# Optimization experiments

Measured on AMD Instinct MI355X. Metric: run time of the kernel, lower is better.

## Reference

```python
import jax, jax.numpy as jnp
import numpy as np

H, DH = 8, 16  # num_heads, head_dim (out_feats // num_heads)
NP, NA, NS = 100000, 60000, 1000


def _gat_conv(feat_src, feat_dst, n_dst, src, dst, W, al, ar, b):
    # DGL GATConv (eval mode: feat_drop/attn_drop are identity)
    hs = (feat_src @ W).reshape(-1, H, DH)          # [Ns,H,D]
    hd = (feat_dst @ W).reshape(-1, H, DH)          # [Nd,H,D]
    el = (hs * al).sum(-1)                          # [Ns,H]
    er = (hd * ar).sum(-1)                          # [Nd,H]
    e = jax.nn.leaky_relu(el[src] + er[dst], negative_slope=0.2)  # [E,H]
    # segment softmax over edges sharing a destination node
    emax = jax.ops.segment_max(e, dst, num_segments=n_dst)
    emax = jnp.where(jnp.isfinite(emax), emax, 0.0)
    ee = jnp.exp(e - emax[dst])
    denom = jax.ops.segment_sum(ee, dst, num_segments=n_dst)
    alpha = ee / jnp.maximum(denom[dst], 1e-9)      # [E,H]
    m = jax.ops.segment_sum(alpha[:, :, None] * hs[src], dst, num_segments=n_dst)
    return m.reshape(n_dst, H * DH) + b             # [Nd, out_feats]


def setup_inputs() -> dict:
    key = jax.random.key(0)
    ks = jax.random.split(key, 18)
    Epa, Eps = 300000, 150000
    f32 = jnp.float32
    inp = {
        "feat_paper_0": jax.random.normal(ks[0], (NP, 128), f32),
        "feat_author_0": jax.random.normal(ks[1], (NA, 128), f32),
        "feat_subject_0": jax.random.normal(ks[2], (NS, 128), f32),
        "feat_paper_1": jax.random.normal(ks[3], (NP, 128), f32),
        "feat_author_1": jax.random.normal(ks[4], (NA, 128), f32),
        "feat_subject_1": jax.random.normal(ks[5], (NS, 128), f32),
        "pa_src": jax.random.randint(ks[6], (Epa,), 0, NP, jnp.int32),
        "pa_dst": jax.random.randint(ks[7], (Epa,), 0, NA, jnp.int32),
        "ap_src": jax.random.randint(ks[8], (Epa,), 0, NA, jnp.int32),
        "ap_dst": jax.random.randint(ks[9], (Epa,), 0, NP, jnp.int32),
        "ps_src": jax.random.randint(ks[10], (Eps,), 0, NP, jnp.int32),
        "ps_dst": jax.random.randint(ks[11], (Eps,), 0, NS, jnp.int32),
        "sp_src": jax.random.randint(ks[12], (Eps,), 0, NS, jnp.int32),
        "sp_dst": jax.random.randint(ks[13], (Eps,), 0, NP, jnp.int32),
        "Ws": jax.random.normal(ks[14], (4, 128, 128), f32) * 0.08,
        "als": jax.random.normal(ks[15], (4, H, DH), f32) * 0.1,
        "ars": jax.random.normal(ks[16], (4, H, DH), f32) * 0.1,
        "bs": jnp.zeros((4, 128), f32),
    }
    return inp


def reference(feat_paper_0, feat_author_0, feat_subject_0,
              feat_paper_1, feat_author_1, feat_subject_1,
              pa_src, pa_dst, ap_src, ap_dst, ps_src, ps_dst, sp_src, sp_dst,
              Ws, als, ars, bs):
    def one_input(fp, fa, fs):
        # rel 0: paper->author, 1: author->paper, 2: paper->subject, 3: subject->paper
        h_author = _gat_conv(fp, fa, NA, pa_src, pa_dst, Ws[0], als[0], ars[0], bs[0])
        h_paper_ap = _gat_conv(fa, fp, NP, ap_src, ap_dst, Ws[1], als[1], ars[1], bs[1])
        h_subject = _gat_conv(fp, fs, NS, ps_src, ps_dst, Ws[2], als[2], ars[2], bs[2])
        h_paper_sp = _gat_conv(fs, fp, NP, sp_src, sp_dst, Ws[3], als[3], ars[3], bs[3])
        h_paper = (h_paper_ap + h_paper_sp) * 0.5  # HeteroGraphConv aggregate='mean'
        # act = identity; key order for ACM: [paper, author, subject]
        return jnp.concatenate([h_paper, h_author, h_subject], axis=0)

    out0 = one_input(feat_paper_0, feat_author_0, feat_subject_0)
    out1 = one_input(feat_paper_1, feat_author_1, feat_subject_1)
    return jnp.stack([out0, out1], axis=0)  # [2, NP+NA+NS, 128]
```

## Files before the change

### kernel.cpp

```cpp
#include <hip/hip_runtime.h>

#define NHEAD 8
#define NPAPER 100000
#define NAUTHOR 60000
#define NSUBJ 1000
#define NTOT (NPAPER + NAUTHOR + NSUBJ)
#define NDEG 261000

typedef __attribute__((ext_vector_type(8))) short bf16x8;
typedef __attribute__((ext_vector_type(4))) float f32x4;

__device__ __forceinline__ unsigned short f2bf(float x) {
    unsigned int u = __builtin_bit_cast(unsigned int, x);
    u += 0x7fffu + ((u >> 16) & 1u);
    return (unsigned short)(u >> 16);
}
__device__ __forceinline__ float bf2f_lo(unsigned int v) {
    return __builtin_bit_cast(float, v << 16);
}
__device__ __forceinline__ float bf2f_hi(unsigned int v) {
    return __builtin_bit_cast(float, v & 0xffff0000u);
}

__global__ void prep_kernel(const float* __restrict__ Ws, const float* __restrict__ als,
                            const float* __restrict__ ars,
                            unsigned short* __restrict__ Wt,
                            unsigned short* __restrict__ combo, int* __restrict__ deg) {
    int b = blockIdx.x;
    if (b >= 288) {
        int idx = (b - 288) * 1024 + threadIdx.x * 4;
        if (idx < NDEG) *reinterpret_cast<int4*>(&deg[idx]) = int4{0, 0, 0, 0};
        return;
    }
    int idx = b * 256 + threadIdx.x;
    if (idx < 65536) {
        int r = idx >> 14, rem = idx & 16383, c = rem >> 7, k = rem & 127;
        Wt[idx] = f2bf(Ws[(r << 14) + k * 128 + c]);
    } else if (idx < 65536 + 8192) {
        int j = idx - 65536;
        int r = j >> 11, rem = j & 2047, n = rem >> 7, k = rem & 127;
        int p = r ^ 1;
        const float *W, *a;
        if (n < 8) {
            W = Ws + (r << 14) + k * 128 + n * 16;
            a = als + r * 128 + n * 16;
        } else {
            int h = n - 8;
            W = Ws + (p << 14) + k * 128 + h * 16;
            a = ars + p * 128 + h * 16;
        }
        float s = 0.f;
#pragma unroll
        for (int d = 0; d < 16; ++d) s += W[d] * a[d];
        combo[j] = f2bf(s);
    }
}

__device__ __forceinline__ void stage_W(unsigned short* Wl, const unsigned short* Wt,
                                        const unsigned short* cb, int tid) {
#pragma unroll
    for (int it = 0; it < 9; ++it) {
        int id = it * 256 + tid;
        int r = id >> 4, c8 = id & 15;
        const unsigned short* srcp = (r < 128) ? (Wt + r * 128) : (cb + (r - 128) * 128);
        uint4 v = *reinterpret_cast<const uint4*>(srcp + c8 * 8);
        *reinterpret_cast<uint4*>(&Wl[(r * 16 + (c8 ^ (r & 15))) * 8]) = v;
    }
}

__device__ __forceinline__ void mfma_set(const unsigned short* Wl, unsigned short* Abf,
                                         const bf16x8* af, int tid, int row0, int N,
                                         float* __restrict__ el, float* __restrict__ er) {
    const int l = tid & 63, w = tid >> 6, lrow = l & 15, lk8 = l >> 4;
#pragma unroll
    for (int t9 = 0; t9 < 9; ++t9) {
        f32x4 acc = f32x4{0.f, 0.f, 0.f, 0.f};
#pragma unroll
        for (int ks = 0; ks < 4; ++ks) {
            int wrow = t9 * 16 + lrow;
            int c8 = ks * 4 + lk8;
            bf16x8 bf = *reinterpret_cast<const bf16x8*>(
                &Wl[(wrow * 16 + (c8 ^ (wrow & 15))) * 8]);
            acc = __builtin_amdgcn_mfma_f32_16x16x32_bf16(af[ks], bf, acc, 0, 0, 0);
        }
        if (t9 < 8) {
#pragma unroll
            for (int r = 0; r < 4; ++r) {
                int rl = w * 16 + lk8 * 4 + r;
                int col = t9 * 16 + lrow;
                Abf[(rl * 16 + ((col >> 3) ^ (rl & 15))) * 8 + (col & 7)] = f2bf(acc[r]);
            }
        } else {
#pragma unroll
            for (int r = 0; r < 4; ++r) {
                int row = row0 + w * 16 + lk8 * 4 + r;
                if (row < N) {
                    if (lrow < 8) el[(size_t)row * 8 + lrow] = acc[r];
                    else er[(size_t)row * 8 + (lrow - 8)] = acc[r];
                }
            }
        }
    }
}

__device__ __forceinline__ void store_hs(const unsigned short* Abf,
                                         unsigned short* __restrict__ hs, int tid,
                                         int row0, int N) {
#pragma unroll
    for (int it = 0; it < 4; ++it) {
        int id = it * 256 + tid;
        int r = id >> 4, c8 = id & 15;
        int row = row0 + r;
        if (row < N) {
            uint4 v = *reinterpret_cast<const uint4*>(&Abf[(r * 16 + (c8 ^ (r & 15))) * 8]);
            *reinterpret_cast<uint4*>(hs + (size_t)row * 128 + c8 * 8) = v;
        }
    }
}

struct PCArgs {
    const int* edst[4];
    int ebase[5];
    int nbase[4];
    int* deg;
    int cblk;
    const float* A[6];
    int N[6];
    int blk0[7];
    const unsigned short* Wt1[6];
    const unsigned short* cb1[6];
    unsigned short* hs1[6];
    float* el1[6];
    float* er1[6];
    const unsigned short* Wt2[6];
    const unsigned short* cb2[6];
    unsigned short* hs2[6];
    float* el2[6];
    float* er2[6];
    int has2[6];
};

__global__ __launch_bounds__(256) void project_count(PCArgs a) {
    __shared__ unsigned short Abf[64 * 128];
    __shared__ unsigned short Wl[144 * 128];
    int bb = blockIdx.x;
    const int tid = threadIdx.x;
    if (bb < a.cblk) {
        int idx = bb * 256 + tid;
        if (idx < a.ebase[4]) {
            int r = 0;
            while (idx >= a.ebase[r + 1]) ++r;
            atomicAdd(&a.deg[a.nbase[r] + a.edst[r][idx - a.ebase[r]]], 1);
        }
        return;
    }
    bb -= a.cblk;
    int t = 0;
    while (bb >= a.blk0[t + 1]) ++t;
    const int row0 = (bb - a.blk0[t]) * 64;
    const int N = a.N[t];
    const float* A = a.A[t];

#pragma unroll
    for (int it = 0; it < 4; ++it) {
        int id = it * 256 + tid;
        int r = id >> 4, c8 = id & 15;
        int row = row0 + r;
        if (row >= N) row = N - 1;
        const float4* ap = reinterpret_cast<const float4*>(A + (size_t)row * 128 + c8 * 8);
        float4 v0 = ap[0], v1 = ap[1];
        uint4 pk;
        pk.x = (unsigned)f2bf(v0.x) | ((unsigned)f2bf(v0.y) << 16);
        pk.y = (unsigned)f2bf(v0.z) | ((unsigned)f2bf(v0.w) << 16);
        pk.z = (unsigned)f2bf(v1.x) | ((unsigned)f2bf(v1.y) << 16);
        pk.w = (unsigned)f2bf(v1.z) | ((unsigned)f2bf(v1.w) << 16);
        *reinterpret_cast<uint4*>(&Abf[(r * 16 + (c8 ^ (r & 15))) * 8]) = pk;
    }
    stage_W(Wl, a.Wt1[t], a.cb1[t], tid);
    __syncthreads();

    const int l = tid & 63, w = tid >> 6, lrow = l & 15, lk8 = l >> 4;
    bf16x8 af[4];
    const int arow = w * 16 + lrow;
#pragma unroll
    for (int ks = 0; ks < 4; ++ks) {
        int c8 = ks * 4 + lk8;
        af[ks] = *reinterpret_cast<const bf16x8*>(
            &Abf[(arow * 16 + (c8 ^ (arow & 15))) * 8]);
    }
    __syncthreads();

    mfma_set(Wl, Abf, af, tid, row0, N, a.el1[t], a.er1[t]);
    __syncthreads();
    store_hs(Abf, a.hs1[t], tid, row0, N);
    if (!a.has2[t]) return;
    stage_W(Wl, a.Wt2[t], a.cb2[t], tid);
    __syncthreads();
    mfma_set(Wl, Abf, af, tid, row0, N, a.el2[t], a.er2[t]);
    __syncthreads();
    store_hs(Abf, a.hs2[t], tid, row0, N);
}

__global__ __launch_bounds__(256) void scan_bsum(const int* __restrict__ deg,
                                                 int* __restrict__ bsums, int N) {
    int base = blockIdx.x * 1024 + threadIdx.x * 4;
    int s = 0;
#pragma unroll
    for (int j = 0; j < 4; ++j) {
        int i = base + j;
        if (i < N) s += deg[i];
    }
#pragma unroll
    for (int off = 32; off; off >>= 1) s += __shfl_down(s, off);
    __shared__ int wt[4];
    if ((threadIdx.x & 63) == 0) wt[threadIdx.x >> 6] = s;
    __syncthreads();
    if (threadIdx.x == 0) bsums[blockIdx.x] = wt[0] + wt[1] + wt[2] + wt[3];
}

__global__ __launch_bounds__(256) void scan_final(const int* __restrict__ deg,
                                                  const int* __restrict__ bsums,
                                                  int* __restrict__ row_ptr,
                                                  int* __restrict__ cursor, int N) {
    int t = threadIdx.x;
    __shared__ int s_start;
    __shared__ int wsum[4];
    {
        int acc = 0;
        for (int i = t; i < (int)blockIdx.x; i += 256) acc += bsums[i];
#pragma unroll
        for (int off = 32; off; off >>= 1) acc += __shfl_down(acc, off);
        if ((t & 63) == 0) wsum[t >> 6] = acc;
        __syncthreads();
        if (t == 0) s_start = wsum[0] + wsum[1] + wsum[2] + wsum[3];
        __syncthreads();
    }
    int base = blockIdx.x * 1024 + t * 4;
    int d[4];
    int s = 0;
#pragma unroll
    for (int j = 0; j < 4; ++j) {
        int i = base + j;
        d[j] = (i < N) ? deg[i] : 0;
        s += d[j];
    }
    int inc = s;
#pragma unroll
    for (int off = 1; off < 64; off <<= 1) {
        int u = __shfl_up(inc, off);
        if ((t & 63) >= off) inc += u;
    }
    __shared__ int wt[4];
    if ((t & 63) == 63) wt[t >> 6] = inc;
    __syncthreads();
    int start = s_start;
    for (int w = 0; w < (t >> 6); ++w) start += wt[w];
    start += inc - s;
#pragma unroll
    for (int j = 0; j < 4; ++j) {
        int i = base + j;
        if (i < N) {
            row_ptr[i] = start;
            cursor[i] = start;
        }
        start += d[j];
    }
    if (base < N && base + 4 >= N) row_ptr[N] = start;
}

struct CsrPtrs {
    const int* esrc[4];
    const int* edst[4];
    int ebase[5];
    int nbase[4];
};

__global__ void csr_scatter(CsrPtrs cp, int* __restrict__ cursor,
                            int* __restrict__ srcs) {
    int idx = blockIdx.x * 256 + threadIdx.x;
    if (idx >= cp.ebase[4]) return;
    int r = 0;
    while (idx >= cp.ebase[r + 1]) ++r;
    int e = idx - cp.ebase[r];
    int p = atomicAdd(&cursor[cp.nbase[r] + cp.edst[r][e]], 1);
    srcs[p] = cp.esrc[r][e];
}

__device__ __forceinline__ void acc_list(int p0, int p1, float erd, int l, int h,
                                         const int* __restrict__ srcs,
                                         const float* __restrict__ el,
                                         const unsigned short* __restrict__ hs,
                                         float* A, float& DS) {
    float a4[4][8];
    float dv[4] = {0.f, 0.f, 0.f, 0.f};
#pragma unroll
    for (int u = 0; u < 4; ++u)
#pragma unroll
        for (int j = 0; j < 8; ++j) a4[u][j] = 0.f;
    int p = p0;
    for (; p + 4 <= p1; p += 4) {
        int sx[4];
#pragma unroll
        for (int u = 0; u < 4; ++u) sx[u] = srcs[p + u];
        float ev[4];
        uint4 q[4];
#pragma unroll
        for (int u = 0; u < 4; ++u) {
            ev[u] = el[(size_t)sx[u] * 8 + h] + erd;
            q[u] = *reinterpret_cast<const uint4*>(hs + (size_t)sx[u] * 128 + l * 8);
        }
#pragma unroll
        for (int u = 0; u < 4; ++u) {
            float e = ev[u];
            e = e > 0.f ? e : 0.2f * e;
            float ee = __expf(e);
            dv[u] += ee;
            a4[u][0] += ee * bf2f_lo(q[u].x);
            a4[u][1] += ee * bf2f_hi(q[u].x);
            a4[u][2] += ee * bf2f_lo(q[u].y);
            a4[u][3] += ee * bf2f_hi(q[u].y);
            a4[u][4] += ee * bf2f_lo(q[u].z);
            a4[u][5] += ee * bf2f_hi(q[u].z);
            a4[u][6] += ee * bf2f_lo(q[u].w);
            a4[u][7] += ee * bf2f_hi(q[u].w);
        }
    }
    for (; p < p1; ++p) {
        int s = srcs[p];
        float e = el[(size_t)s * 8 + h] + erd;
        e = e > 0.f ? e : 0.2f * e;
        float ee = __expf(e);
        uint4 q = *reinterpret_cast<const uint4*>(hs + (size_t)s * 128 + l * 8);
        dv[0] += ee;
        a4[0][0] += ee * bf2f_lo(q.x);
        a4[0][1] += ee * bf2f_hi(q.x);
        a4[0][2] += ee * bf2f_lo(q.y);
        a4[0][3] += ee * bf2f_hi(q.y);
        a4[0][4] += ee * bf2f_lo(q.z);
        a4[0][5] += ee * bf2f_hi(q.z);
        a4[0][6] += ee * bf2f_lo(q.w);
        a4[0][7] += ee * bf2f_hi(q.w);
    }
#pragma unroll
    for (int j = 0; j < 8; ++j) A[j] = a4[0][j] + a4[1][j] + a4[2][j] + a4[3][j];
    DS = dv[0] + dv[1] + dv[2] + dv[3];
}

#define PB 12500
#define AB 7500
#define SB 2000

struct AggArgs {
    const int* rp;
    const int* srcs;
    const float* el[8];
    const float* er[8];
    const unsigned short* hs[8];
    const float* bs;
    float* out0;
    float* out1;
};

__global__ __launch_bounds__(256) void mega_agg(AggArgs a) {
    int blk = blockIdx.x;
    __shared__ float Am[16][128];
    __shared__ float Dm[16][8];

    if (blk < PB) {
        int g = blk * 16 + (threadIdx.x >> 4);
        int l = threadIdx.x & 15, h = l >> 1;
        int inp = g >= NPAPER;
        int dst = inp ? g - NPAPER : g;
        float* out = (inp ? a.out1 : a.out0) + (size_t)dst * 128 + l * 8;
        float A1[8], A3[8], d1, d3;
        acc_list(a.rp[60000 + dst], a.rp[60000 + dst + 1],
                 a.er[inp * 4 + 1][(size_t)dst * 8 + h], l, h, a.srcs,
                 a.el[inp * 4 + 1], a.hs[inp * 4 + 1], A1, d1);
        acc_list(a.rp[161000 + dst], a.rp[161000 + dst + 1],
                 a.er[inp * 4 + 3][(size_t)dst * 8 + h], l, h, a.srcs,
                 a.el[inp * 4 + 3], a.hs[inp * 4 + 3], A3, d3);
        float i1 = 1.f / fmaxf(d1, 1e-9f);
        float i3 = 1.f / fmaxf(d3, 1e-9f);
        const float4* bp1 = reinterpret_cast<const float4*>(a.bs + 128 + l * 8);
        const float4* bp3 = reinterpret_cast<const float4*>(a.bs + 384 + l * 8);
        float4 b10 = bp1[0], b11 = bp1[1], b30 = bp3[0], b31 = bp3[1];
        float4 o0, o1;
        o0.x = 0.5f * ((A1[0] * i1 + b10.x) + (A3[0] * i3 + b30.x));
        o0.y = 0.5f * ((A1[1] * i1 + b10.y) + (A3[1] * i3 + b30.y));
        o0.z = 0.5f * ((A1[2] * i1 + b10.z) + (A3[2] * i3 + b30.z));
        o0.w = 0.5f * ((A1[3] * i1 + b10.w) + (A3[3] * i3 + b30.w));
        o1.x = 0.5f * ((A1[4] * i1 + b11.x) + (A3[4] * i3 + b31.x));
        o1.y = 0.5f * ((A1[5] * i1 + b11.y) + (A3[5] * i3 + b31.y));
        o1.z = 0.5f * ((A1[6] * i1 + b11.z) + (A3[6] * i3 + b31.z));
        o1.w = 0.5f * ((A1[7] * i1 + b11.w) + (A3[7] * i3 + b31.w));
        reinterpret_cast<float4*>(out)[0] = o0;
        reinterpret_cast<float4*>(out)[1] = o1;
    } else if (blk < PB + AB) {
        int g = (blk - PB) * 16 + (threadIdx.x >> 4);
        int l = threadIdx.x & 15, h = l >> 1;
        int inp = g >= NAUTHOR;
        int dst = inp ? g - NAUTHOR : g;
        float* out = (inp ? a.out1 : a.out0) + (size_t)(NPAPER + dst) * 128 + l * 8;
        float A[8], ds;
        acc_list(a.rp[dst], a.rp[dst + 1], a.er[inp * 4 + 0][(size_t)dst * 8 + h], l, h,
                 a.srcs, a.el[inp * 4 + 0], a.hs[inp * 4 + 0], A, ds);
        float inv = 1.f / fmaxf(ds, 1e-9f);
        const float4* bp = reinterpret_cast<const float4*>(a.bs + l * 8);
        float4 b0 = bp[0], b1 = bp[1];
        float4 o0 = make_float4(A[0] * inv + b0.x, A[1] * inv + b0.y,
                                A[2] * inv + b0.z, A[3] * inv + b0.w);
        float4 o1 = make_float4(A[4] * inv + b1.x, A[5] * inv + b1.y,
                                A[6] * inv + b1.z, A[7] * inv + b1.w);
        reinterpret_cast<float4*>(out)[0] = o0;
        reinterpret_cast<float4*>(out)[1] = o1;
    } else {
        int b2 = blk - (PB + AB);
        int inp = b2 >= NSUBJ;
        int dst = inp ? b2 - NSUBJ : b2;
        const float* el = a.el[inp * 4 + 2];
        const float* er = a.er[inp * 4 + 2];
        const unsigned short* hs = a.hs[inp * 4 + 2];
        float* out = (inp ? a.out1 : a.out0) + (size_t)(NPAPER + NAUTHOR + dst) * 128;
        int gl = threadIdx.x >> 4;
        int l = threadIdx.x & 15, h = l >> 1;
        int p0 = a.rp[160000 + dst], p1 = a.rp[160000 + dst + 1];
        float erd = er[(size_t)dst * 8 + h];
        float acc8[8];
#pragma unroll
        for (int j = 0; j < 8; ++j) acc8[j] = 0.f;
        float dsum = 0.f;
        for (int p = p0 + gl; p < p1; p += 16) {
            int s = a.srcs[p];
            float e = el[(size_t)s * 8 + h] + erd;
            e = e > 0.f ? e : 0.2f * e;
            float ee = __expf(e);
            uint4 q = *reinterpret_cast<const uint4*>(hs + (size_t)s * 128 + l * 8);
            dsum += ee;
            acc8[0] += ee * bf2f_lo(q.x);
            acc8[1] += ee * bf2f_hi(q.x);
            acc8[2] += ee * bf2f_lo(q.y);
            acc8[3] += ee * bf2f_hi(q.y);
            acc8[4] += ee * bf2f_lo(q.z);
            acc8[5] += ee * bf2f_hi(q.z);
            acc8[6] += ee * bf2f_lo(q.w);
            acc8[7] += ee * bf2f_hi(q.w);
        }
#pragma unroll
        for (int j = 0; j < 8; ++j) Am[gl][l * 8 + j] = acc8[j];
        if ((l & 1) == 0) Dm[gl][h] = dsum;
        __syncthreads();
        int c = threadIdx.x;
        if (c < 128) {
            float s = 0.f, dn = 0.f;
            int hh = c >> 4;
#pragma unroll
            for (int g = 0; g < 16; ++g) {
                s += Am[g][c];
                dn += Dm[g][hh];
            }
            out[c] = s / fmaxf(dn, 1e-9f) + a.bs[256 + c];
        }
    }
}

extern "C" void kernel_launch(void* const* d_in, const int* in_sizes, int n_in,
                              void* d_out, int out_size, void* d_ws, size_t ws_size,
                              hipStream_t stream) {
    const float* Ws4 = (const float*)d_in[14];
    const float* als = (const float*)d_in[15];
    const float* ars = (const float*)d_in[16];
    const float* bs = (const float*)d_in[17];
    float* out = (float*)d_out;

    const int Es[4] = {in_sizes[6], in_sizes[8], in_sizes[10], in_sizes[12]};
    const int Nsrcs[4] = {NPAPER, NAUTHOR, NPAPER, NSUBJ};
    const int Ndsts[4] = {NAUTHOR, NPAPER, NSUBJ, NPAPER};
    const int Etot = Es[0] + Es[1] + Es[2] + Es[3];

    char* wsp = (char*)d_ws;
    auto carve = [&](size_t bytes) {
        char* p = wsp;
        wsp += (bytes + 255) & ~(size_t)255;
        return p;
    };
    unsigned short* Wt = (unsigned short*)carve(4 * 16384 * 2);
    unsigned short* combo = (unsigned short*)carve(4 * 2048 * 2);
    unsigned short* hsb[2][4];
    float* elb[2][4];
    float* erb[2][4];
    for (int i = 0; i < 2; ++i)
        for (int r = 0; r < 4; ++r) {
            hsb[i][r] = (unsigned short*)carve((size_t)Nsrcs[r] * 128 * 2);
            elb[i][r] = (float*)carve((size_t)Nsrcs[r] * 8 * 4);
            erb[i][r] = (float*)carve((size_t)Ndsts[r] * 8 * 4);
        }
    int* deg = (int*)carve((size_t)NDEG * 4);
    int* cursor = (int*)carve((size_t)NDEG * 4);
    int* bsums = (int*)carve(1024);
    int* rp = (int*)carve((size_t)(NDEG + 1) * 4);
    int* scsr = (int*)carve((size_t)Etot * 4);

    prep_kernel<<<288 + (NDEG + 1023) / 1024, 256, 0, stream>>>(Ws4, als, ars, Wt,
                                                                combo, deg);

    PCArgs pc;
    pc.edst[0] = (const int*)d_in[7];
    pc.edst[1] = (const int*)d_in[9];
    pc.edst[2] = (const int*)d_in[11];
    pc.edst[3] = (const int*)d_in[13];
    pc.ebase[0] = 0;
    for (int r = 0; r < 4; ++r) pc.ebase[r + 1] = pc.ebase[r] + Es[r];
    pc.nbase[0] = 0;
    pc.nbase[1] = 60000;
    pc.nbase[2] = 160000;
    pc.nbase[3] = 161000;
    pc.deg = deg;
    pc.cblk = (Etot + 255) / 256;

    int blk = 0;
    for (int ti = 0; ti < 6; ++ti) {
        int i = ti & 1;
        int nodeT = ti >> 1;
        const int relOf[3] = {0, 1, 3};
        int r = relOf[nodeT];
        const float* feats[3] = {(const float*)d_in[0 + 3 * i],
                                 (const float*)d_in[1 + 3 * i],
                                 (const float*)d_in[2 + 3 * i]};
        pc.A[ti] = feats[nodeT];
        pc.N[ti] = (nodeT == 0) ? NPAPER : (nodeT == 1 ? NAUTHOR : NSUBJ);
        pc.blk0[ti] = blk;
        blk += (pc.N[ti] + 63) / 64;
        pc.Wt1[ti] = Wt + (size_t)r * 16384;
        pc.cb1[ti] = combo + (size_t)r * 2048;
        pc.hs1[ti] = hsb[i][r];
        pc.el1[ti] = elb[i][r];
        pc.er1[ti] = erb[i][r ^ 1];
        pc.has2[ti] = (nodeT == 0);
        int r2 = 2;
        pc.Wt2[ti] = Wt + (size_t)r2 * 16384;
        pc.cb2[ti] = combo + (size_t)r2 * 2048;
        pc.hs2[ti] = hsb[i][r2];
        pc.el2[ti] = elb[i][r2];
        pc.er2[ti] = erb[i][r2 ^ 1];
    }
    pc.blk0[6] = blk;
    project_count<<<pc.cblk + blk, 256, 0, stream>>>(pc);

    int nb = (NDEG + 1023) / 1024;
    scan_bsum<<<nb, 256, 0, stream>>>(deg, bsums, NDEG);
    scan_final<<<nb, 256, 0, stream>>>(deg, bsums, rp, cursor, NDEG);

    CsrPtrs cp;
    cp.esrc[0] = (const int*)d_in[6];  cp.edst[0] = (const int*)d_in[7];
    cp.esrc[1] = (const int*)d_in[8];  cp.edst[1] = (const int*)d_in[9];
    cp.esrc[2] = (const int*)d_in[10]; cp.edst[2] = (const int*)d_in[11];
    cp.esrc[3] = (const int*)d_in[12]; cp.edst[3] = (const int*)d_in[13];
    for (int r = 0; r < 5; ++r) cp.ebase[r] = pc.ebase[r];
    for (int r = 0; r < 4; ++r) cp.nbase[r] = pc.nbase[r];
    csr_scatter<<<(Etot + 255) / 256, 256, 0, stream>>>(cp, cursor, scsr);

    AggArgs ag;
    ag.rp = rp;
    ag.srcs = scsr;
    for (int i = 0; i < 2; ++i)
        for (int r = 0; r < 4; ++r) {
            ag.el[i * 4 + r] = elb[i][r];
            ag.er[i * 4 + r] = erb[i][r];
            ag.hs[i * 4 + r] = hsb[i][r];
        }
    ag.bs = bs;
    ag.out0 = out;
    ag.out1 = out + (size_t)NTOT * 128;
    mega_agg<<<PB + AB + SB, 256, 0, stream>>>(ag);
}
```

Measured before the change: 384.0 us.

## Process both inputs per destination in one pass sharing CSR source indices

The aggregation kernel now handles inputs 0 and 1 together for each destination node, so each CSR source index and row pointer is loaded once and feeds two gathers. The unroll-by-4 partial accumulators are replaced with two accumulator sets, one per input. The subject path splits the block into two 8-group halves, one per input, and the block count is halved. Non-temporal loads and stores are added for feature reads and output writes. More loads are in flight per thread, but the kernel now uses more registers and each accumulator has fewer independent chains.

```diff
diff --git a/kernel.cpp b/kernel.cpp
--- a/kernel.cpp
+++ b/kernel.cpp
@@ -9,6 +9,7 @@
 
 typedef __attribute__((ext_vector_type(8))) short bf16x8;
 typedef __attribute__((ext_vector_type(4))) float f32x4;
+typedef __attribute__((ext_vector_type(4))) unsigned int u32x4;
 
 __device__ __forceinline__ unsigned short f2bf(float x) {
     unsigned int u = __builtin_bit_cast(unsigned int, x);
@@ -167,8 +168,9 @@
         int r = id >> 4, c8 = id & 15;
         int row = row0 + r;
         if (row >= N) row = N - 1;
-        const float4* ap = reinterpret_cast<const float4*>(A + (size_t)row * 128 + c8 * 8);
-        float4 v0 = ap[0], v1 = ap[1];
+        const f32x4* ap = reinterpret_cast<const f32x4*>(A + (size_t)row * 128 + c8 * 8);
+        f32x4 v0 = __builtin_nontemporal_load(ap);
+        f32x4 v1 = __builtin_nontemporal_load(ap + 1);
         uint4 pk;
         pk.x = (unsigned)f2bf(v0.x) | ((unsigned)f2bf(v0.y) << 16);
         pk.y = (unsigned)f2bf(v0.z) | ((unsigned)f2bf(v0.w) << 16);
@@ -286,69 +288,102 @@
     srcs[p] = cp.esrc[r][e];
 }
 
-__device__ __forceinline__ void acc_list(int p0, int p1, float erd, int l, int h,
-                                         const int* __restrict__ srcs,
-                                         const float* __restrict__ el,
-                                         const unsigned short* __restrict__ hs,
-                                         float* A, float& DS) {
-    float a4[4][8];
-    float dv[4] = {0.f, 0.f, 0.f, 0.f};
-#pragma unroll
-    for (int u = 0; u < 4; ++u)
-#pragma unroll
-        for (int j = 0; j < 8; ++j) a4[u][j] = 0.f;
+__device__ __forceinline__ void acc_dual(
+    int p0, int p1, float erd0, float erd1, int l, int h,
+    const int* __restrict__ srcs,
+    const float* __restrict__ el0, const float* __restrict__ el1,
+    const unsigned short* __restrict__ hs0, const unsigned short* __restrict__ hs1,
+    float* A0, float* A1, float& DS0, float& DS1) {
+    float a0[8], a1[8];
+#pragma unroll
+    for (int j = 0; j < 8; ++j) { a0[j] = 0.f; a1[j] = 0.f; }
+    float d0 = 0.f, d1 = 0.f;
     int p = p0;
     for (; p + 4 <= p1; p += 4) {
         int sx[4];
 #pragma unroll
         for (int u = 0; u < 4; ++u) sx[u] = srcs[p + u];
-        float ev[4];
-        uint4 q[4];
+        float ev0[4], ev1[4];
+        uint4 q0[4], q1[4];
 #pragma unroll
         for (int u = 0; u < 4; ++u) {
-            ev[u] = el[(size_t)sx[u] * 8 + h] + erd;
-            q[u] = *reinterpret_cast<const uint4*>(hs + (size_t)sx[u] * 128 + l * 8);
+            ev0[u] = el0[(size_t)sx[u] * 8 + h] + erd0;
+            ev1[u] = el1[(size_t)sx[u] * 8 + h] + erd1;
+            q0[u] = *reinterpret_cast<const uint4*>(hs0 + (size_t)sx[u] * 128 + l * 8);
+            q1[u] = *reinterpret_cast<const uint4*>(hs1 + (size_t)sx[u] * 128 + l * 8);
         }
 #pragma unroll
         for (int u = 0; u < 4; ++u) {
-            float e = ev[u];
-            e = e > 0.f ? e : 0.2f * e;
-            float ee = __expf(e);
-            dv[u] += ee;
-            a4[u][0] += ee * bf2f_lo(q[u].x);
-            a4[u][1] += ee * bf2f_hi(q[u].x);
-            a4[u][2] += ee * bf2f_lo(q[u].y);
-            a4[u][3] += ee * bf2f_hi(q[u].y);
-            a4[u][4] += ee * bf2f_lo(q[u].z);
-            a4[u][5] += ee * bf2f_hi(q[u].z);
-            a4[u][6] += ee * bf2f_lo(q[u].w);
-            a4[u][7] += ee * bf2f_hi(q[u].w);
+            float e0 = ev0[u];
+            e0 = e0 > 0.f ? e0 : 0.2f * e0;
+            float ee0 = __expf(e0);
+            d0 += ee0;
+            a0[0] += ee0 * bf2f_lo(q0[u].x);
+            a0[1] += ee0 * bf2f_hi(q0[u].x);
+            a0[2] += ee0 * bf2f_lo(q0[u].y);
+            a0[3] += ee0 * bf2f_hi(q0[u].y);
+            a0[4] += ee0 * bf2f_lo(q0[u].z);
+            a0[5] += ee0 * bf2f_hi(q0[u].z);
+            a0[6] += ee0 * bf2f_lo(q0[u].w);
+            a0[7] += ee0 * bf2f_hi(q0[u].w);
+            float e1 = ev1[u];
+            e1 = e1 > 0.f ? e1 : 0.2f * e1;
+            float ee1 = __expf(e1);
+            d1 += ee1;
+            a1[0] += ee1 * bf2f_lo(q1[u].x);
+            a1[1] += ee1 * bf2f_hi(q1[u].x);
+            a1[2] += ee1 * bf2f_lo(q1[u].y);
+            a1[3] += ee1 * bf2f_hi(q1[u].y);
+            a1[4] += ee1 * bf2f_lo(q1[u].z);
+            a1[5] += ee1 * bf2f_hi(q1[u].z);
+            a1[6] += ee1 * bf2f_lo(q1[u].w);
+            a1[7] += ee1 * bf2f_hi(q1[u].w);
         }
     }
     for (; p < p1; ++p) {
         int s = srcs[p];
-        float e = el[(size_t)s * 8 + h] + erd;
-        e = e > 0.f ? e : 0.2f * e;
-        float ee = __expf(e);
-        uint4 q = *reinterpret_cast<const uint4*>(hs + (size_t)s * 128 + l * 8);
-        dv[0] += ee;
-        a4[0][0] += ee * bf2f_lo(q.x);
-        a4[0][1] += ee * bf2f_hi(q.x);
-        a4[0][2] += ee * bf2f_lo(q.y);
-        a4[0][3] += ee * bf2f_hi(q.y);
-        a4[0][4] += ee * bf2f_lo(q.z);
-        a4[0][5] += ee * bf2f_hi(q.z);
-        a4[0][6] += ee * bf2f_lo(q.w);
-        a4[0][7] += ee * bf2f_hi(q.w);
-    }
-#pragma unroll
-    for (int j = 0; j < 8; ++j) A[j] = a4[0][j] + a4[1][j] + a4[2][j] + a4[3][j];
-    DS = dv[0] + dv[1] + dv[2] + dv[3];
-}
-
-#define PB 12500
-#define AB 7500
-#define SB 2000
+        float e0 = el0[(size_t)s * 8 + h] + erd0;
+        float e1 = el1[(size_t)s * 8 + h] + erd1;
+        uint4 q0 = *reinterpret_cast<const uint4*>(hs0 + (size_t)s * 128 + l * 8);
+        uint4 q1 = *reinterpret_cast<const uint4*>(hs1 + (size_t)s * 128 + l * 8);
+        e0 = e0 > 0.f ? e0 : 0.2f * e0;
+        float ee0 = __expf(e0);
+        d0 += ee0;
+        a0[0] += ee0 * bf2f_lo(q0.x);
+        a0[1] += ee0 * bf2f_hi(q0.x);
+        a0[2] += ee0 * bf2f_lo(q0.y);
+        a0[3] += ee0 * bf2f_hi(q0.y);
+        a0[4] += ee0 * bf2f_lo(q0.z);
+        a0[5] += ee0 * bf2f_hi(q0.z);
+        a0[6] += ee0 * bf2f_lo(q0.w);
+        a0[7] += ee0 * bf2f_hi(q0.w);
+        e1 = e1 > 0.f ? e1 : 0.2f * e1;
+        float ee1 = __expf(e1);
+        d1 += ee1;
+        a1[0] += ee1 * bf2f_lo(q1.x);
+        a1[1] += ee1 * bf2f_hi(q1.x);
+        a1[2] += ee1 * bf2f_lo(q1.y);
+        a1[3] += ee1 * bf2f_hi(q1.y);
+        a1[4] += ee1 * bf2f_lo(q1.z);
+        a1[5] += ee1 * bf2f_hi(q1.z);
+        a1[6] += ee1 * bf2f_lo(q1.w);
+        a1[7] += ee1 * bf2f_hi(q1.w);
+    }
+#pragma unroll
+    for (int j = 0; j < 8; ++j) { A0[j] = a0[j]; A1[j] = a1[j]; }
+    DS0 = d0;
+    DS1 = d1;
+}
+
+__device__ __forceinline__ void nt_store2(float* op, f32x4 o0, f32x4 o1) {
+    f32x4* vp = reinterpret_cast<f32x4*>(op);
+    __builtin_nontemporal_store(o0, vp);
+    __builtin_nontemporal_store(o1, vp + 1);
+}
+
+#define PB2 6250
+#define AB2 3750
+#define SB2 1000
 
 struct AggArgs {
     const int* rp;
@@ -366,70 +401,81 @@
     __shared__ float Am[16][128];
     __shared__ float Dm[16][8];
 
-    if (blk < PB) {
-        int g = blk * 16 + (threadIdx.x >> 4);
+    if (blk < PB2) {
+        int dst = blk * 16 + (threadIdx.x >> 4);
         int l = threadIdx.x & 15, h = l >> 1;
-        int inp = g >= NPAPER;
-        int dst = inp ? g - NPAPER : g;
-        float* out = (inp ? a.out1 : a.out0) + (size_t)dst * 128 + l * 8;
-        float A1[8], A3[8], d1, d3;
-        acc_list(a.rp[60000 + dst], a.rp[60000 + dst + 1],
-                 a.er[inp * 4 + 1][(size_t)dst * 8 + h], l, h, a.srcs,
-                 a.el[inp * 4 + 1], a.hs[inp * 4 + 1], A1, d1);
-        acc_list(a.rp[161000 + dst], a.rp[161000 + dst + 1],
-                 a.er[inp * 4 + 3][(size_t)dst * 8 + h], l, h, a.srcs,
-                 a.el[inp * 4 + 3], a.hs[inp * 4 + 3], A3, d3);
-        float i1 = 1.f / fmaxf(d1, 1e-9f);
-        float i3 = 1.f / fmaxf(d3, 1e-9f);
+        if (dst >= NPAPER) return;
+        float A1_0[8], A1_1[8], d1_0, d1_1;
+        acc_dual(a.rp[60000 + dst], a.rp[60000 + dst + 1],
+                 a.er[1][(size_t)dst * 8 + h], a.er[5][(size_t)dst * 8 + h], l, h,
+                 a.srcs, a.el[1], a.el[5], a.hs[1], a.hs[5], A1_0, A1_1, d1_0, d1_1);
+        float A3_0[8], A3_1[8], d3_0, d3_1;
+        acc_dual(a.rp[161000 + dst], a.rp[161000 + dst + 1],
+                 a.er[3][(size_t)dst * 8 + h], a.er[7][(size_t)dst * 8 + h], l, h,
+                 a.srcs, a.el[3], a.el[7], a.hs[3], a.hs[7], A3_0, A3_1, d3_0, d3_1);
         const float4* bp1 = reinterpret_cast<const float4*>(a.bs + 128 + l * 8);
         const float4* bp3 = reinterpret_cast<const float4*>(a.bs + 384 + l * 8);
         float4 b10 = bp1[0], b11 = bp1[1], b30 = bp3[0], b31 = bp3[1];
-        float4 o0, o1;
-        o0.x = 0.5f * ((A1[0] * i1 + b10.x) + (A3[0] * i3 + b30.x));
-        o0.y = 0.5f * ((A1[1] * i1 + b10.y) + (A3[1] * i3 + b30.y));
-        o0.z = 0.5f * ((A1[2] * i1 + b10.z) + (A3[2] * i3 + b30.z));
-        o0.w = 0.5f * ((A1[3] * i1 + b10.w) + (A3[3] * i3 + b30.w));
-        o1.x = 0.5f * ((A1[4] * i1 + b11.x) + (A3[4] * i3 + b31.x));
-        o1.y = 0.5f * ((A1[5] * i1 + b11.y) + (A3[5] * i3 + b31.y));
-        o1.z = 0.5f * ((A1[6] * i1 + b11.z) + (A3[6] * i3 + b31.z));
-        o1.w = 0.5f * ((A1[7] * i1 + b11.w) + (A3[7] * i3 + b31.w));
-        reinterpret_cast<float4*>(out)[0] = o0;
-        reinterpret_cast<float4*>(out)[1] = o1;
-    } else if (blk < PB + AB) {
-        int g = (blk - PB) * 16 + (threadIdx.x >> 4);
+        float i1 = 1.f / fmaxf(d1_0, 1e-9f);
+        float i3 = 1.f / fmaxf(d3_0, 1e-9f);
+        f32x4 o0, o1;
+        o0.x = 0.5f * ((A1_0[0] * i1 + b10.x) + (A3_0[0] * i3 + b30.x));
+        o0.y = 0.5f * ((A1_0[1] * i1 + b10.y) + (A3_0[1] * i3 + b30.y));
+        o0.z = 0.5f * ((A1_0[2] * i1 + b10.z) + (A3_0[2] * i3 + b30.z));
+        o0.w = 0.5f * ((A1_0[3] * i1 + b10.w) + (A3_0[3] * i3 + b30.w));
+        o1.x = 0.5f * ((A1_0[4] * i1 + b11.x) + (A3_0[4] * i3 + b31.x));
+        o1.y = 0.5f * ((A1_0[5] * i1 + b11.y) + (A3_0[5] * i3 + b31.y));
+        o1.z = 0.5f * ((A1_0[6] * i1 + b11.z) + (A3_0[6] * i3 + b31.z));
+        o1.w = 0.5f * ((A1_0[7] * i1 + b11.w) + (A3_0[7] * i3 + b31.w));
+        nt_store2(a.out0 + (size_t)dst * 128 + l * 8, o0, o1);
+        i1 = 1.f / fmaxf(d1_1, 1e-9f);
+        i3 = 1.f / fmaxf(d3_1, 1e-9f);
+        o0.x = 0.5f * ((A1_1[0] * i1 + b10.x) + (A3_1[0] * i3 + b30.x));
+        o0.y = 0.5f * ((A1_1[1] * i1 + b10.y) + (A3_1[1] * i3 + b30.y));
+        o0.z = 0.5f * ((A1_1[2] * i1 + b10.z) + (A3_1[2] * i3 + b30.z));
+        o0.w = 0.5f * ((A1_1[3] * i1 + b10.w) + (A3_1[3] * i3 + b30.w));
+        o1.x = 0.5f * ((A1_1[4] * i1 + b11.x) + (A3_1[4] * i3 + b31.x));
+        o1.y = 0.5f * ((A1_1[5] * i1 + b11.y) + (A3_1[5] * i3 + b31.y));
+        o1.z = 0.5f * ((A1_1[6] * i1 + b11.z) + (A3_1[6] * i3 + b31.z));
+        o1.w = 0.5f * ((A1_1[7] * i1 + b11.w) + (A3_1[7] * i3 + b31.w));
+        nt_store2(a.out1 + (size_t)dst * 128 + l * 8, o0, o1);
+    } else if (blk < PB2 + AB2) {
+        int dst = (blk - PB2) * 16 + (threadIdx.x >> 4);
         int l = threadIdx.x & 15, h = l >> 1;
-        int inp = g >= NAUTHOR;
-        int dst = inp ? g - NAUTHOR : g;
-        float* out = (inp ? a.out1 : a.out0) + (size_t)(NPAPER + dst) * 128 + l * 8;
-        float A[8], ds;
-        acc_list(a.rp[dst], a.rp[dst + 1], a.er[inp * 4 + 0][(size_t)dst * 8 + h], l, h,
-                 a.srcs, a.el[inp * 4 + 0], a.hs[inp * 4 + 0], A, ds);
-        float inv = 1.f / fmaxf(ds, 1e-9f);
+        if (dst >= NAUTHOR) return;
+        float A0[8], A1[8], d0, d1;
+        acc_dual(a.rp[dst], a.rp[dst + 1],
+                 a.er[0][(size_t)dst * 8 + h], a.er[4][(size_t)dst * 8 + h], l, h,
+                 a.srcs, a.el[0], a.el[4], a.hs[0], a.hs[4], A0, A1, d0, d1);
         const float4* bp = reinterpret_cast<const float4*>(a.bs + l * 8);
         float4 b0 = bp[0], b1 = bp[1];
-        float4 o0 = make_float4(A[0] * inv + b0.x, A[1] * inv + b0.y,
-                                A[2] * inv + b0.z, A[3] * inv + b0.w);
-        float4 o1 = make_float4(A[4] * inv + b1.x, A[5] * inv + b1.y,
-                                A[6] * inv + b1.z, A[7] * inv + b1.w);
-        reinterpret_cast<float4*>(out)[0] = o0;
-        reinterpret_cast<float4*>(out)[1] = o1;
+        float inv = 1.f / fmaxf(d0, 1e-9f);
+        f32x4 o0 = {A0[0] * inv + b0.x, A0[1] * inv + b0.y,
+                    A0[2] * inv + b0.z, A0[3] * inv + b0.w};
+        f32x4 o1 = {A0[4] * inv + b1.x, A0[5] * inv + b1.y,
+                    A0[6] * inv + b1.z, A0[7] * inv + b1.w};
+        nt_store2(a.out0 + (size_t)(NPAPER + dst) * 128 + l * 8, o0, o1);
+        inv = 1.f / fmaxf(d1, 1e-9f);
+        o0 = f32x4{A1[0] * inv + b0.x, A1[1] * inv + b0.y,
+                   A1[2] * inv + b0.z, A1[3] * inv + b0.w};
+        o1 = f32x4{A1[4] * inv + b1.x, A1[5] * inv + b1.y,
+                   A1[6] * inv + b1.z, A1[7] * inv + b1.w};
+        nt_store2(a.out1 + (size_t)(NPAPER + dst) * 128 + l * 8, o0, o1);
     } else {
-        int b2 = blk - (PB + AB);
-        int inp = b2 >= NSUBJ;
-        int dst = inp ? b2 - NSUBJ : b2;
+        int dst = blk - (PB2 + AB2);
+        int gl = threadIdx.x >> 4;
+        int inp = gl >> 3, ck = gl & 7;
+        int l = threadIdx.x & 15, h = l >> 1;
         const float* el = a.el[inp * 4 + 2];
         const float* er = a.er[inp * 4 + 2];
         const unsigned short* hs = a.hs[inp * 4 + 2];
-        float* out = (inp ? a.out1 : a.out0) + (size_t)(NPAPER + NAUTHOR + dst) * 128;
-        int gl = threadIdx.x >> 4;
-        int l = threadIdx.x & 15, h = l >> 1;
         int p0 = a.rp[160000 + dst], p1 = a.rp[160000 + dst + 1];
         float erd = er[(size_t)dst * 8 + h];
         float acc8[8];
 #pragma unroll
         for (int j = 0; j < 8; ++j) acc8[j] = 0.f;
         float dsum = 0.f;
-        for (int p = p0 + gl; p < p1; p += 16) {
+        for (int p = p0 + ck; p < p1; p += 8) {
             int s = a.srcs[p];
             float e = el[(size_t)s * 8 + h] + erd;
             e = e > 0.f ? e : 0.2f * e;
@@ -450,16 +496,18 @@
         if ((l & 1) == 0) Dm[gl][h] = dsum;
         __syncthreads();
         int c = threadIdx.x;
-        if (c < 128) {
-            float s = 0.f, dn = 0.f;
-            int hh = c >> 4;
-#pragma unroll
-            for (int g = 0; g < 16; ++g) {
-                s += Am[g][c];
-                dn += Dm[g][hh];
-            }
-            out[c] = s / fmaxf(dn, 1e-9f) + a.bs[256 + c];
-        }
+        int ci = c >> 7;
+        int col = c & 127;
+        float s = 0.f, dn = 0.f;
+        int hh = col >> 4;
+#pragma unroll
+        for (int g = 0; g < 8; ++g) {
+            s += Am[ci * 8 + g][col];
+            dn += Dm[ci * 8 + g][hh];
+        }
+        float v = s / fmaxf(dn, 1e-9f) + a.bs[256 + col];
+        float* outp = (ci ? a.out1 : a.out0) + (size_t)(NPAPER + NAUTHOR + dst) * 128 + col;
+        __builtin_nontemporal_store(v, outp);
     }
 }
 
@@ -571,5 +619,5 @@
     ag.bs = bs;
     ag.out0 = out;
     ag.out1 = out + (size_t)NTOT * 128;
-    mega_agg<<<PB + AB + SB, 256, 0, stream>>>(ag);
-}
+    mega_agg<<<PB2 + AB2 + SB2, 256, 0, stream>>>(ag);
+}
```

Result: faster. 324.5 us (-15.5%).
